# Optimization experiments

Measured on AMD Instinct MI355X. Metric: run time of the kernel, lower is better.

## Reference

```python
import jax, jax.numpy as jnp
import numpy as np


def setup_inputs() -> dict:
    key = jax.random.key(0)
    ks = jax.random.split(key, 8)
    T, B, D = 2048, 8, 1024
    d, NM, k = 64, 8, 2
    Mp1 = NM + 1
    s_in = 1.0 / np.sqrt(D)
    X = jax.random.normal(ks[0], (T, B, D), dtype=jnp.float32)
    M0 = 0.02 * jax.random.normal(ks[1], (d, d), dtype=jnp.float32)
    W_q = s_in * jax.random.normal(ks[2], (D, d), dtype=jnp.float32)
    b_q = jnp.zeros((d,), jnp.float32)
    W_k = s_in * jax.random.normal(ks[3], (D, Mp1 * d), dtype=jnp.float32)
    b_k = jnp.zeros((Mp1 * d,), jnp.float32)
    W_v = s_in * jax.random.normal(ks[4], (D, Mp1 * d), dtype=jnp.float32)
    b_v = jnp.zeros((Mp1 * d,), jnp.float32)
    W_g = s_in * jax.random.normal(ks[5], (D, NM), dtype=jnp.float32)
    b_g = jnp.zeros((NM,), jnp.float32)
    return dict(X=X, M0=M0, W_q=W_q, b_q=b_q, W_k=W_k, b_k=b_k,
                W_v=W_v, b_v=b_v, W_g=W_g, b_g=b_g, k=k)


def _mom_forward(X, M0, W_q, b_q, W_k, b_k, W_v, b_v, W_g, b_g, k):
    T, B, D = X.shape
    d = M0.shape[0]
    NM = W_g.shape[1]
    Mp1 = NM + 1  # memory 0 is the always-on shared memory
    Kp1 = k + 1
    # --- gating + top-k memory selection ---
    scores = jax.nn.softmax(X @ W_g + b_g, axis=-1)               # (T,B,NM)
    m_sc, m_idx = jax.lax.top_k(scores, k)                        # (T,B,k)
    m_sc = m_sc / jnp.sum(m_sc, axis=-1, keepdims=True)
    m_idx = m_idx + 1                                             # shift: 0 reserved for shared memory
    idx_u = jnp.concatenate([jnp.zeros((T, B, 1), m_idx.dtype), m_idx], axis=2)  # (T,B,Kp1)
    sc_u = jnp.concatenate([jnp.ones((T, B, 1), m_sc.dtype), m_sc], axis=2)      # (T,B,Kp1)
    # --- varlen pack: sort replicated tokens by (batch, memory, time) ---
    # NB: the torch build_varlen_pack runs under @torch.no_grad -> detached
    t_rep = jnp.broadcast_to(jnp.arange(T)[:, None, None], (T, B, Kp1)).reshape(-1)
    b_rep = jnp.broadcast_to(jnp.arange(B)[None, :, None], (T, B, Kp1)).reshape(-1)
    m_rep = idx_u.reshape(-1)
    sort_key = b_rep * (Mp1 * T) + m_rep * T + t_rep              # unique per packed token
    perm = jnp.argsort(sort_key)
    t_o = t_rep[perm]
    b_o = b_rep[perm]
    m_id = m_rep[perm]
    alpha = jax.lax.stop_gradient(sc_u.reshape(-1)[perm])         # (Tt,)
    x_tilde = jax.lax.stop_gradient(
        jnp.broadcast_to(X[:, :, None, :], (T, B, Kp1, D)).reshape(-1, D)[perm])  # (Tt,D)
    Tt = T * B * Kp1
    # segment id per packed token; state resets at each new (batch, memory) segment
    seg = b_o * Mp1 + m_id
    new_seg = jnp.concatenate([jnp.ones((1,), bool), seg[1:] != seg[:-1]])
    # --- projections; pick k/v head matching each token's routed memory ---
    q_t = x_tilde @ W_q + b_q                                     # (Tt,d)
    K_all = (x_tilde @ W_k + b_k).reshape(Tt, Mp1, d)
    V_all = (x_tilde @ W_v + b_v).reshape(Tt, Mp1, d)
    k_t = jnp.take_along_axis(K_all, m_id[:, None, None], axis=1)[:, 0]  # (Tt,d)
    v_t = jnp.take_along_axis(V_all, m_id[:, None, None], axis=1)[:, 0]  # (Tt,d)
    # --- per-segment linear-attention recurrence: M_t = M0 + sum k_tau v_tau^T, o_t = q_t @ M_t ---
    def step(M, inp):
        qt, kt, vt, ns = inp
        M = jnp.where(ns, M0, M)
        M = M + kt[:, None] * vt[None, :]
        return M, qt @ M
    _, o_tilde = jax.lax.scan(step, M0, (q_t, k_t, v_t, new_seg))  # (Tt,d)
    # --- weighted scatter-add back to (T,B,d) ---
    o = jnp.zeros((T, B, d), X.dtype).at[t_o, b_o].add(alpha[:, None] * o_tilde)
    return o


def reference(X, M0, W_q, b_q, W_k, b_k, W_v, b_v, W_g, b_g, k):
    return _mom_forward(X, M0, W_q, b_q, W_k, b_k, W_v, b_v, W_g, b_g, k)
```

## Files before the change

kernel.cpp:

```cpp
#include <hip/hip_runtime.h>

#define TT   2048
#define BB   8
#define DD   1024
#define HD   64
#define MP1  9
#define NTOK (TT*BB)
#define CH   64
#define NC   32
#define NSEG (BB*MP1)
#define SEGCAP 2048
#define NCAT 1280
#define LDP  72
#define NZB  1024

typedef __attribute__((ext_vector_type(8))) short bf16x8;
typedef __attribute__((ext_vector_type(4))) float f32x4;

union U8 { uint4 v; unsigned short s[8]; };

static __device__ __forceinline__ unsigned short f2bf(float f) {
  union { float f; unsigned u; } c; c.f = f;
  unsigned r = (c.u + 0x7FFF + ((c.u >> 16) & 1)) >> 16;
  return (unsigned short)r;
}
static __device__ __forceinline__ float bf2f(unsigned short s) {
  union { unsigned u; float f; } c; c.u = ((unsigned)s) << 16;
  return c.f;
}

static __device__ __forceinline__ int sched_walk(
    const int* __restrict__ seglen, int bid, int* chunk_out) {
  const int batch = bid & 7;
  int idx = bid >> 3;
  for (int m = 0; m < MP1; m++) {
    int nch = (seglen[batch * MP1 + m] + 63) >> 6;
    if (idx < nch) { *chunk_out = idx; return batch * MP1 + m; }
    idx -= nch;
  }
  return -1;
}

__global__ __launch_bounds__(256) void prep(
    const float* __restrict__ X,
    const float* __restrict__ Wq, const float* __restrict__ Wk,
    const float* __restrict__ Wv, const float* __restrict__ bq,
    const float* __restrict__ bk, const float* __restrict__ bv,
    const float* __restrict__ Wg, const float* __restrict__ bg,
    unsigned short* __restrict__ Wt, float* __restrict__ bcat,
    int2* __restrict__ idxb, float2* __restrict__ alfb,
    unsigned short* __restrict__ Xb,
    float4* __restrict__ outz, int n4) {
  __shared__ float smem[8 * DD];
  const int tid = threadIdx.x;
  const int id = blockIdx.x;
  if (id >= 1344) {
    int i = (id - 1344) * 256 + tid;
    if (i < n4) outz[i] = make_float4(0.f, 0.f, 0.f, 0.f);
    return;
  }
  if (id < 320) {
    float (*tile)[65] = (float(*)[65])smem;
    const int n0 = (id % 20) * 64, k0 = (id / 20) * 64;
    const int c = tid & 63, rr = tid >> 6;
#pragma unroll 4
    for (int i = 0; i < 16; i++) {
      int kk = k0 + rr * 16 + i;
      int n  = n0 + c;
      float v = 0.f;
      if (n0 < 64)        v = Wq[kk * 64 + n];
      else if (n0 < 640)  v = Wk[kk * 576 + (n - 64)];
      else if (n0 < 1216) v = Wv[kk * 576 + (n - 640)];
      tile[rr * 16 + i][c] = v;
    }
    __syncthreads();
    const int lk = (tid & 15) * 4, ln = tid >> 4;
#pragma unroll
    for (int p = 0; p < 4; p++) {
      int nl = p * 16 + ln;
      ushort4 o;
      o.x = f2bf(tile[lk + 0][nl]); o.y = f2bf(tile[lk + 1][nl]);
      o.z = f2bf(tile[lk + 2][nl]); o.w = f2bf(tile[lk + 3][nl]);
      *(ushort4*)&Wt[(size_t)(n0 + nl) * DD + k0 + lk] = o;
    }
    if (id == 0) {
      for (int idx = tid; idx < NCAT; idx += 256) {
        float b = 0.f;
        if (idx < 64)        b = bq[idx];
        else if (idx < 640)  b = bk[idx - 64];
        else if (idx < 1216) b = bv[idx - 640];
        bcat[idx] = b;
      }
    }
    return;
  }
  float* wgT = smem;
#pragma unroll
  for (int idx4 = tid; idx4 < 2048; idx4 += 256) {
    float4 v = *(const float4*)&Wg[(size_t)idx4 * 4];
    int flat = idx4 * 4;
    int i = flat >> 3, j = flat & 7;
    wgT[(j + 0) * DD + i] = v.x;
    wgT[(j + 1) * DD + i] = v.y;
    wgT[(j + 2) * DD + i] = v.z;
    wgT[(j + 3) * DD + i] = v.w;
  }
  __syncthreads();
  const int lane = tid & 63, wave = tid >> 6;
  const int base_tok = (id - 320) * 16 + wave * 4;
  for (int tk = 0; tk < 4; tk++) {
    const int tok = base_tok + tk;
    const float* xr = X + (size_t)tok * DD;
    unsigned short* xbr = Xb + ((size_t)((tok & 7) * TT + (tok >> 3))) * DD;
    float p[8] = {0.f,0.f,0.f,0.f,0.f,0.f,0.f,0.f};
#pragma unroll
    for (int it = 0; it < 4; it++) {
      int i = it * 256 + lane * 4;
      float4 x = *(const float4*)&xr[i];
      ushort4 o;
      o.x = f2bf(x.x); o.y = f2bf(x.y); o.z = f2bf(x.z); o.w = f2bf(x.w);
      *(ushort4*)&xbr[i] = o;
#pragma unroll
      for (int j = 0; j < 8; j++) {
        float4 wv = *(const float4*)&wgT[j * DD + i];
        p[j] += x.x * wv.x + x.y * wv.y + x.z * wv.z + x.w * wv.w;
      }
    }
#pragma unroll
    for (int j = 0; j < 8; j++) {
      float v = p[j];
#pragma unroll
      for (int off = 32; off > 0; off >>= 1) v += __shfl_xor(v, off);
      p[j] = v + bg[j];
    }
    if (lane == 0) {
      int i1 = 0; float z1 = p[0];
#pragma unroll
      for (int j = 1; j < 8; j++) if (p[j] > z1) { z1 = p[j]; i1 = j; }
      int i2 = -1; float z2 = -3.0e38f;
#pragma unroll
      for (int j = 0; j < 8; j++) if (j != i1 && p[j] > z2) { z2 = p[j]; i2 = j; }
      float e   = expf(z2 - z1);
      float inv = 1.0f / (1.0f + e);
      idxb[tok] = make_int2(i1 + 1, i2 + 1);
      alfb[tok] = make_float2(inv, e * inv);
    }
  }
}

__global__ __launch_bounds__(1024) void pack_kernel(
    const int2* __restrict__ idxb, const float2* __restrict__ alfb,
    int* __restrict__ tlist, float* __restrict__ alist,
    int* __restrict__ seglen) {
  const int seg = blockIdx.x;
  const int b = seg / MP1, m = seg % MP1;
  const int tid = threadIdx.x;
  int* tl = tlist + (size_t)seg * SEGCAP;
  float* al = alist + (size_t)seg * SEGCAP;
  if (m == 0) {
    for (int pos = tid; pos < TT; pos += 1024) { tl[pos] = pos; al[pos] = 1.f; }
    if (tid == 0) seglen[seg] = TT;
    return;
  }
  __shared__ int wsum[16];
  const int lane = tid & 63, w = tid >> 6;
  int base = 0;
  for (int r = 0; r < TT / 1024; r++) {
    int t = r * 1024 + tid;
    int2 ix = idxb[t * BB + b];
    bool f = (ix.x == m || ix.y == m);
    float2 af = alfb[t * BB + b];
    float alpha = (ix.x == m) ? af.x : af.y;
    unsigned long long mask = __ballot(f);
    int lanepos = __popcll(mask & ((1ull << lane) - 1ull));
    if (lane == 0) wsum[w] = __popcll(mask);
    __syncthreads();
    int wbase = 0, total = 0;
#pragma unroll
    for (int i = 0; i < 16; i++) { int v = wsum[i]; if (i < w) wbase += v; total += v; }
    if (f) { int pos = base + wbase + lanepos; tl[pos] = t; al[pos] = alpha; }
    base += total;
    __syncthreads();
  }
  if (tid == 0) seglen[seg] = base;
  int Lpad = (base + 63) & ~63;
  for (int pos = base + tid; pos < Lpad; pos += 1024) { tl[pos] = 0; al[pos] = 0.f; }
}

#define ABUF_H 4096
#define BBUF_H 12288

__global__ __launch_bounds__(256) void pkv_intra(
    const unsigned short* __restrict__ Xb, const unsigned short* __restrict__ Wt,
    const float* __restrict__ bcat,
    const int* __restrict__ tlist, const float* __restrict__ alist,
    const int* __restrict__ seglen,
    unsigned short* __restrict__ Sb16, unsigned short* __restrict__ Qd,
    float* __restrict__ out) {
  int chunk;
  const int seg = sched_walk(seglen, blockIdx.x, &chunk);
  if (seg < 0) return;
  const int t0 = chunk * 64;
  const int L = seglen[seg];
  const int b = seg / MP1, m = seg % MP1;
  __shared__ unsigned short lds[2 * (ABUF_H + BBUF_H)];
  __shared__ int tls[64];
  unsigned short* Asb = lds;
  unsigned short* Bsb = lds + 2 * ABUF_H;
  const int tid = threadIdx.x;
  const int lane = tid & 63, w = tid >> 6;
  if (tid < 64) tls[tid] = tlist[(size_t)seg * SEGCAP + t0 + tid];
  __syncthreads();

  const int lrow = lane >> 2;
  const int lk = (((lane & 3) ^ ((lane >> 3) & 3))) * 8;
  const unsigned short* aPtr = Xb + ((size_t)b * TT + tls[w * 16 + lrow]) * DD + lk;
  const unsigned short* kPtr = Wt + (size_t)(64  + m * 64 + w * 16 + lrow) * DD + lk;
  const unsigned short* vPtr = Wt + (size_t)(640 + m * 64 + w * 16 + lrow) * DD + lk;
  const unsigned short* qPtr = Wt + (size_t)(w * 16 + lrow) * DD + lk;

  const int wr = (w >> 1) * 32;
  const int wc64 = (w & 1);
  const int quad = lane >> 4, l15 = lane & 15;
  const int qs = quad ^ ((l15 >> 1) & 3);

  float biasv[4], qbias[2];
#pragma unroll
  for (int n = 0; n < 4; n++) {
    int col = wc64 * 64 + n * 16 + l15;
    biasv[n] = bcat[col < 64 ? (64 + m * 64 + col) : (640 + m * 64 + (col - 64))];
  }
#pragma unroll
  for (int i = 0; i < 2; i++) qbias[i] = bcat[wc64 * 32 + i * 16 + l15];
  asm volatile("s_waitcnt vmcnt(0)" ::: "memory");
  __builtin_amdgcn_sched_barrier(0);

  f32x4 acc[2][4];
  f32x4 qacc[2][2];
#pragma unroll
  for (int i = 0; i < 2; i++) {
#pragma unroll
    for (int j = 0; j < 4; j++) acc[i][j] = (f32x4){0.f, 0.f, 0.f, 0.f};
#pragma unroll
    for (int j = 0; j < 2; j++) qacc[i][j] = (f32x4){0.f, 0.f, 0.f, 0.f};
  }

#define STG(BUF, K0)                                                             \
  do {                                                                           \
    unsigned short* As_ = Asb + (BUF) * ABUF_H;                                  \
    unsigned short* Bs_ = Bsb + (BUF) * BBUF_H;                                  \
    _Pragma("unroll")                                                            \
    for (int s = 0; s < 2; s++) {                                                \
      __builtin_amdgcn_global_load_lds(                                          \
          (const __attribute__((address_space(1))) unsigned int*)(aPtr + (K0) + s * 32), \
          (__attribute__((address_space(3))) unsigned int*)(As_ + s * 2048 + w * 512),   \
          16, 0, 0);                                                             \
      __builtin_amdgcn_global_load_lds(                                          \
          (const __attribute__((address_space(1))) unsigned int*)(kPtr + (K0) + s * 32), \
          (__attribute__((address_space(3))) unsigned int*)(Bs_ + s * 2048 + w * 512),   \
          16, 0, 0);                                                             \
      __builtin_amdgcn_global_load_lds(                                          \
          (const __attribute__((address_space(1))) unsigned int*)(vPtr + (K0) + s * 32), \
          (__attribute__((address_space(3))) unsigned int*)(Bs_ + 4096 + s * 2048 + w * 512), \
          16, 0, 0);                                                             \
      __builtin_amdgcn_global_load_lds(                                          \
          (const __attribute__((address_space(1))) unsigned int*)(qPtr + (K0) + s * 32), \
          (__attribute__((address_space(3))) unsigned int*)(Bs_ + 8192 + s * 2048 + w * 512), \
          16, 0, 0);                                                             \
    }                                                                            \
  } while (0)

#define CMP(BUF)                                                                 \
  do {                                                                           \
    const unsigned short* As_ = Asb + (BUF) * ABUF_H;                            \
    const unsigned short* Bs_ = Bsb + (BUF) * BBUF_H;                            \
    _Pragma("unroll")                                                            \
    for (int s = 0; s < 2; s++) {                                                \
      bf16x8 af[2], bfr[4];                                                      \
      _Pragma("unroll")                                                          \
      for (int i = 0; i < 2; i++)                                                \
        af[i] = *(const bf16x8*)&As_[s * 2048 + (wr + i * 16 + l15) * 32 + qs * 8]; \
      _Pragma("unroll")                                                          \
      for (int n = 0; n < 4; n++)                                                \
        bfr[n] = *(const bf16x8*)&Bs_[wc64 * 4096 + s * 2048 + (n * 16 + l15) * 32 + qs * 8]; \
      _Pragma("unroll")                                                          \
      for (int mi = 0; mi < 2; mi++)                                             \
        _Pragma("unroll")                                                        \
        for (int ni = 0; ni < 4; ni++)                                           \
          acc[mi][ni] = __builtin_amdgcn_mfma_f32_16x16x32_bf16(af[mi], bfr[ni], acc[mi][ni], 0, 0, 0); \
      {                                                                          \
        bf16x8 qf[2];                                                            \
        _Pragma("unroll")                                                        \
        for (int i = 0; i < 2; i++)                                              \
          qf[i] = *(const bf16x8*)&Bs_[8192 + s * 2048 + (wc64 * 32 + i * 16 + l15) * 32 + qs * 8]; \
        _Pragma("unroll")                                                        \
        for (int mi = 0; mi < 2; mi++)                                           \
          _Pragma("unroll")                                                      \
          for (int ni = 0; ni < 2; ni++)                                         \
            qacc[mi][ni] = __builtin_amdgcn_mfma_f32_16x16x32_bf16(af[mi], qf[ni], qacc[mi][ni], 0, 0, 0); \
      }                                                                          \
    }                                                                            \
  } while (0)

  STG(0, 0);
  STG(1, 64);
  for (int it = 0; it < 15; it++) {
    asm volatile("s_waitcnt vmcnt(8)" ::: "memory");
    __builtin_amdgcn_sched_barrier(0);
    asm volatile("s_barrier" ::: "memory");
    CMP(it & 1);
    asm volatile("s_waitcnt lgkmcnt(0)" ::: "memory");
    __builtin_amdgcn_sched_barrier(0);
    asm volatile("s_barrier" ::: "memory");
    if (it < 14) STG(it & 1, (it + 2) * 64);
  }
  asm volatile("s_waitcnt vmcnt(0)" ::: "memory");
  __builtin_amdgcn_sched_barrier(0);
  asm volatile("s_barrier" ::: "memory");
  CMP(1);
#undef STG
#undef CMP

  asm volatile("s_waitcnt lgkmcnt(0)" ::: "memory");
  __builtin_amdgcn_sched_barrier(0);
  __syncthreads();

  unsigned short* Qs  = lds;
  unsigned short* Ks  = lds + 64 * LDP;
  unsigned short* KTs = lds + 2 * 64 * LDP;
  unsigned short* VTs = lds + 3 * 64 * LDP;

#pragma unroll
  for (int ni = 0; ni < 2; ni++) {
    int qcol = wc64 * 32 + ni * 16 + l15;
#pragma unroll
    for (int mi = 0; mi < 2; mi++) {
#pragma unroll
      for (int r = 0; r < 4; r++) {
        int pr = wr + mi * 16 + quad * 4 + r;
        unsigned short qv = f2bf(qacc[mi][ni][r] + qbias[ni]);
        Qs[pr * LDP + qcol] = qv;
        if (m == 0) Qd[(size_t)((t0 + pr) * BB + b) * HD + qcol] = qv;
      }
    }
  }
#pragma unroll
  for (int ni = 0; ni < 4; ni++) {
    int col = ni * 16 + l15;
#pragma unroll
    for (int mi = 0; mi < 2; mi++) {
#pragma unroll
      for (int r = 0; r < 4; r++) {
        int pr = wr + mi * 16 + quad * 4 + r;
        unsigned short v = f2bf(acc[mi][ni][r] + biasv[ni]);
        if (wc64 == 0) {
          unsigned short kv = (t0 + pr < L) ? v : (unsigned short)0;
          Ks[pr * LDP + col]  = kv;
          KTs[col * LDP + pr] = kv;
        } else {
          VTs[col * LDP + pr] = v;
        }
      }
    }
  }
  __syncthreads();

  const int* tl = tlist + (size_t)seg * SEGCAP;
  {
    const unsigned short* arow = &VTs[(w * 16 + l15) * LDP];
    bf16x8 a0 = *(const bf16x8*)(arow + quad * 8);
    bf16x8 a1 = *(const bf16x8*)(arow + 32 + quad * 8);
    unsigned short* Sp = Sb16 + ((size_t)seg * NC + chunk) * 4096;
#pragma unroll
    for (int n = 0; n < 4; n++) {
      const unsigned short* brow = &KTs[(n * 16 + l15) * LDP];
      f32x4 a2 = __builtin_amdgcn_mfma_f32_16x16x32_bf16(a0, *(const bf16x8*)(brow + quad * 8),
                                                         (f32x4){0.f,0.f,0.f,0.f}, 0, 0, 0);
      a2 = __builtin_amdgcn_mfma_f32_16x16x32_bf16(a1, *(const bf16x8*)(brow + 32 + quad * 8),
                                                   a2, 0, 0, 0);
#pragma unroll
      for (int r = 0; r < 4; r++)
        Sp[(w * 16 + quad * 4 + r) * 64 + n * 16 + l15] = f2bf(a2[r]);
    }
  }
  unsigned short* qrow = &Qs[(w * 16 + l15) * LDP];
  bf16x8 aq0 = *(const bf16x8*)(qrow + quad * 8);
  bf16x8 aq1 = *(const bf16x8*)(qrow + 32 + quad * 8);
  f32x4 pp[4];
#pragma unroll
  for (int n = 0; n < 4; n++) {
    const unsigned short* krow = &Ks[(n * 16 + l15) * LDP];
    pp[n] = __builtin_amdgcn_mfma_f32_16x16x32_bf16(aq0, *(const bf16x8*)(krow + quad * 8),
                                                    (f32x4){0.f,0.f,0.f,0.f}, 0, 0, 0);
    pp[n] = __builtin_amdgcn_mfma_f32_16x16x32_bf16(aq1, *(const bf16x8*)(krow + 32 + quad * 8),
                                                    pp[n], 0, 0, 0);
  }
#pragma unroll
  for (int n = 0; n < 4; n++)
#pragma unroll
    for (int r = 0; r < 4; r++) {
      int i = w * 16 + quad * 4 + r, j = n * 16 + l15;
      Qs[i * LDP + j] = (j <= i) ? f2bf(pp[n][r]) : (unsigned short)0;
    }
  bf16x8 ap0 = *(const bf16x8*)(qrow + quad * 8);
  bf16x8 ap1 = *(const bf16x8*)(qrow + 32 + quad * 8);
  f32x4 po[4];
#pragma unroll
  for (int n = 0; n < 4; n++) {
    const unsigned short* vrow = &VTs[(n * 16 + l15) * LDP];
    po[n] = __builtin_amdgcn_mfma_f32_16x16x32_bf16(ap0, *(const bf16x8*)(vrow + quad * 8),
                                                    (f32x4){0.f,0.f,0.f,0.f}, 0, 0, 0);
    po[n] = __builtin_amdgcn_mfma_f32_16x16x32_bf16(ap1, *(const bf16x8*)(vrow + 32 + quad * 8),
                                                    po[n], 0, 0, 0);
  }
#pragma unroll
  for (int r = 0; r < 4; r++) {
    int pos = t0 + w * 16 + quad * 4 + r;
    if (pos < L) {
      int t = tl[pos];
      float alpha = alist[(size_t)seg * SEGCAP + pos];
#pragma unroll
      for (int n = 0; n < 4; n++)
        atomicAdd(&out[(size_t)(t * BB + b) * HD + n * 16 + l15], alpha * po[n][r]);
    }
  }
}

__global__ __launch_bounds__(256) void scan_kernel(
    const float* __restrict__ M0, const int* __restrict__ seglen,
    unsigned short* __restrict__ Sb16) {
  const int batch = blockIdx.x & 7;
  const int idx = blockIdx.x >> 3;
  const int seg = batch * MP1 + (idx >> 2), slab = idx & 3;
  const int nch = (seglen[seg] + CH - 1) / CH;
  if (nch <= 0) return;
  const int tid = threadIdx.x;
  const int off = slab * 1024 + tid * 4;
  float run[4];
#pragma unroll
  for (int u = 0; u < 4; u++) {
    int o = off + u;
    run[u] = M0[(o & 63) * 64 + (o >> 6)];
  }
  unsigned short* base = Sb16 + (size_t)seg * NC * 4096;
  ushort4 s = *(const ushort4*)(base + off);
  for (int c = 0; c < nch; c++) {
    unsigned short* p = base + c * 4096 + off;
    ushort4 snext;
    if (c + 1 < nch) snext = *(const ushort4*)(p + 4096);
    ushort4 o;
    o.x = f2bf(run[0]); o.y = f2bf(run[1]); o.z = f2bf(run[2]); o.w = f2bf(run[3]);
    *(ushort4*)p = o;
    run[0] += bf2f(s.x); run[1] += bf2f(s.y); run[2] += bf2f(s.z); run[3] += bf2f(s.w);
    s = snext;
  }
}

__global__ __launch_bounds__(256) void chunk_inter(
    const unsigned short* __restrict__ Qd, const unsigned short* __restrict__ Sb16,
    const int* __restrict__ tlist, const float* __restrict__ alist,
    const int* __restrict__ seglen, float* __restrict__ out) {
  int chunk;
  const int seg = sched_walk(seglen, blockIdx.x, &chunk);
  if (seg < 0) return;
  const int L = seglen[seg];
  const int t0 = chunk * CH;
  __shared__ unsigned short Qs[64 * LDP];
  __shared__ unsigned short MT[64 * LDP];
  const int b = seg / MP1;
  const int tid = threadIdx.x;
  const int* tl = tlist + (size_t)seg * SEGCAP;
  {
    int row = tid >> 2, c16 = (tid & 3) << 4;
    int pos = t0 + row;
    const unsigned short* qb = Qd + (size_t)(tl[pos] * BB + b) * HD;
    *(uint4*)&Qs[row * LDP + c16]     = *(const uint4*)(qb + c16);
    *(uint4*)&Qs[row * LDP + c16 + 8] = *(const uint4*)(qb + c16 + 8);
    const unsigned short* Mp = Sb16 + ((size_t)seg * NC + chunk) * 4096 + row * 64 + c16;
    *(uint4*)&MT[row * LDP + c16]     = *(const uint4*)(Mp);
    *(uint4*)&MT[row * LDP + c16 + 8] = *(const uint4*)(Mp + 8);
  }
  __syncthreads();
  const int lane = tid & 63, w = tid >> 6;
  const int quad = lane >> 4, l15 = lane & 15;
  const unsigned short* qrow = &Qs[(w * 16 + l15) * LDP];
  bf16x8 aq0 = *(const bf16x8*)(qrow + quad * 8);
  bf16x8 aq1 = *(const bf16x8*)(qrow + 32 + quad * 8);
  f32x4 po[4];
#pragma unroll
  for (int n = 0; n < 4; n++) {
    const unsigned short* mrow = &MT[(n * 16 + l15) * LDP];
    po[n] = __builtin_amdgcn_mfma_f32_16x16x32_bf16(aq0, *(const bf16x8*)(mrow + quad * 8),
                                                    (f32x4){0.f,0.f,0.f,0.f}, 0, 0, 0);
    po[n] = __builtin_amdgcn_mfma_f32_16x16x32_bf16(aq1, *(const bf16x8*)(mrow + 32 + quad * 8),
                                                    po[n], 0, 0, 0);
  }
#pragma unroll
  for (int r = 0; r < 4; r++) {
    int pos = t0 + w * 16 + quad * 4 + r;
    if (pos < L) {
      int t = tl[pos];
      float alpha = alist[(size_t)seg * SEGCAP + pos];
#pragma unroll
      for (int n = 0; n < 4; n++)
        atomicAdd(&out[(size_t)(t * BB + b) * HD + n * 16 + l15], alpha * po[n][r]);
    }
  }
}

extern "C" void kernel_launch(void* const* d_in, const int* in_sizes, int n_in,
                              void* d_out, int out_size, void* d_ws, size_t ws_size,
                              hipStream_t stream) {
  const float* X  = (const float*)d_in[0];
  const float* M0 = (const float*)d_in[1];
  const float* Wq = (const float*)d_in[2];
  const float* bq = (const float*)d_in[3];
  const float* Wk = (const float*)d_in[4];
  const float* bk = (const float*)d_in[5];
  const float* Wv = (const float*)d_in[6];
  const float* bv = (const float*)d_in[7];
  const float* Wg = (const float*)d_in[8];
  const float* bg = (const float*)d_in[9];

  char* ws = (char*)d_ws;
  unsigned short* Xb   = (unsigned short*)(ws);
  unsigned short* Wt   = (unsigned short*)(ws + 33554432ULL);
  float*          bcat = (float*)         (ws + 36175872ULL);
  unsigned short* Qd   = (unsigned short*)(ws + 36180992ULL);
  unsigned short* Sb16 = (unsigned short*)(ws + 76026880ULL);
  int2*           idxb = (int2*)          (ws + 94901248ULL);
  float2*         alfb = (float2*)        (ws + 95032320ULL);
  int*            tlist= (int*)           (ws + 95163392ULL);
  float*          alist= (float*)         (ws + 95753216ULL);
  int*            slen = (int*)           (ws + 96343040ULL);

  float* out = (float*)d_out;
  const int n4 = out_size / 4;

  prep<<<320 + NTOK / 16 + NZB, 256, 0, stream>>>(
      X, Wq, Wk, Wv, bq, bk, bv, Wg, bg, Wt, bcat, idxb, alfb, Xb,
      (float4*)out, n4);
  pack_kernel<<<NSEG, 1024, 0, stream>>>(idxb, alfb, tlist, alist, slen);
  pkv_intra<<<1024, 256, 0, stream>>>(Xb, Wt, bcat, tlist, alist, slen, Sb16, Qd, out);
  scan_kernel<<<288, 256, 0, stream>>>(M0, slen, Sb16);
  chunk_inter<<<1024, 256, 0, stream>>>(Qd, Sb16, tlist, alist, slen, out);
}
```

Baseline: 110.9 us.

## Double pkv_intra block to 512 threads, splitting GEMM rows across eight waves

Launches the projection/intra-chunk kernel with 8 waves instead of 4. Each wave now computes a 16-row slice of the K/V/Q projection instead of 32 rows. Each wave also stages one of the four source arrays (X, K, V or Q weights) into shared memory, and the vmcnt wait drops to match the smaller number of loads in flight per wave. The intra-chunk attention epilogue stays on the first four waves. This halves per-wave accumulator registers and raises the number of waves available to hide latency, at the cost of idle waves in the epilogue and more barrier participants.

```diff
diff --git a/kernel.cpp b/kernel.cpp
--- a/kernel.cpp
+++ b/kernel.cpp
@@ -190,7 +190,7 @@
 #define ABUF_H 4096
 #define BBUF_H 12288
 
-__global__ __launch_bounds__(256) void pkv_intra(
+__global__ __launch_bounds__(512) void pkv_intra(
     const unsigned short* __restrict__ Xb, const unsigned short* __restrict__ Wt,
     const float* __restrict__ bcat,
     const int* __restrict__ tlist, const float* __restrict__ alist,
@@ -212,17 +212,26 @@
   if (tid < 64) tls[tid] = tlist[(size_t)seg * SEGCAP + t0 + tid];
   __syncthreads();
 
-  const int lrow = lane >> 2;
-  const int lk = (((lane & 3) ^ ((lane >> 3) & 3))) * 8;
-  const unsigned short* aPtr = Xb + ((size_t)b * TT + tls[w * 16 + lrow]) * DD + lk;
-  const unsigned short* kPtr = Wt + (size_t)(64  + m * 64 + w * 16 + lrow) * DD + lk;
-  const unsigned short* vPtr = Wt + (size_t)(640 + m * 64 + w * 16 + lrow) * DD + lk;
-  const unsigned short* qPtr = Wt + (size_t)(w * 16 + lrow) * DD + lk;
-
-  const int wr = (w >> 1) * 32;
-  const int wc64 = (w & 1);
+  const int arr = w >> 1;
+  const int sl  = w & 1;
+  const int lk  = (((lane & 3) ^ ((lane >> 3) & 3))) * 8;
+  const unsigned short* src[4];
+#pragma unroll
+  for (int i = 0; i < 4; i++) {
+    int row = i * 16 + (lane >> 2);
+    const unsigned short* p;
+    if (arr == 0)      p = Xb + ((size_t)b * TT + tls[row]) * DD;
+    else if (arr == 1) p = Wt + (size_t)(64  + m * 64 + row) * DD;
+    else if (arr == 2) p = Wt + (size_t)(640 + m * 64 + row) * DD;
+    else               p = Wt + (size_t)(row) * DD;
+    src[i] = p + sl * 32 + lk;
+  }
+  const int dstoff = (arr == 0) ? (sl * 2048) : ((arr - 1) * 4096 + sl * 2048);
+
+  const int wrB  = (w >> 1) * 16;
+  const int wc64 = w & 1;
   const int quad = lane >> 4, l15 = lane & 15;
-  const int qs = quad ^ ((l15 >> 1) & 3);
+  const int qs   = quad ^ ((l15 >> 1) & 3);
 
   float biasv[4], qbias[2];
 #pragma unroll
@@ -235,39 +244,23 @@
   asm volatile("s_waitcnt vmcnt(0)" ::: "memory");
   __builtin_amdgcn_sched_barrier(0);
 
-  f32x4 acc[2][4];
-  f32x4 qacc[2][2];
-#pragma unroll
-  for (int i = 0; i < 2; i++) {
-#pragma unroll
-    for (int j = 0; j < 4; j++) acc[i][j] = (f32x4){0.f, 0.f, 0.f, 0.f};
-#pragma unroll
-    for (int j = 0; j < 2; j++) qacc[i][j] = (f32x4){0.f, 0.f, 0.f, 0.f};
-  }
+  f32x4 acc[4];
+  f32x4 qacc[2];
+#pragma unroll
+  for (int j = 0; j < 4; j++) acc[j] = (f32x4){0.f, 0.f, 0.f, 0.f};
+#pragma unroll
+  for (int j = 0; j < 2; j++) qacc[j] = (f32x4){0.f, 0.f, 0.f, 0.f};
 
 #define STG(BUF, K0)                                                             \
   do {                                                                           \
-    unsigned short* As_ = Asb + (BUF) * ABUF_H;                                  \
-    unsigned short* Bs_ = Bsb + (BUF) * BBUF_H;                                  \
+    unsigned short* db = ((arr == 0) ? (Asb + (BUF) * ABUF_H)                    \
+                                     : (Bsb + (BUF) * BBUF_H)) + dstoff;         \
     _Pragma("unroll")                                                            \
-    for (int s = 0; s < 2; s++) {                                                \
+    for (int i = 0; i < 4; i++)                                                  \
       __builtin_amdgcn_global_load_lds(                                          \
-          (const __attribute__((address_space(1))) unsigned int*)(aPtr + (K0) + s * 32), \
-          (__attribute__((address_space(3))) unsigned int*)(As_ + s * 2048 + w * 512),   \
+          (const __attribute__((address_space(1))) unsigned int*)(src[i] + (K0)),\
+          (__attribute__((address_space(3))) unsigned int*)(db + i * 512),       \
           16, 0, 0);                                                             \
-      __builtin_amdgcn_global_load_lds(                                          \
-          (const __attribute__((address_space(1))) unsigned int*)(kPtr + (K0) + s * 32), \
-          (__attribute__((address_space(3))) unsigned int*)(Bs_ + s * 2048 + w * 512),   \
-          16, 0, 0);                                                             \
-      __builtin_amdgcn_global_load_lds(                                          \
-          (const __attribute__((address_space(1))) unsigned int*)(vPtr + (K0) + s * 32), \
-          (__attribute__((address_space(3))) unsigned int*)(Bs_ + 4096 + s * 2048 + w * 512), \
-          16, 0, 0);                                                             \
-      __builtin_amdgcn_global_load_lds(                                          \
-          (const __attribute__((address_space(1))) unsigned int*)(qPtr + (K0) + s * 32), \
-          (__attribute__((address_space(3))) unsigned int*)(Bs_ + 8192 + s * 2048 + w * 512), \
-          16, 0, 0);                                                             \
-    }                                                                            \
   } while (0)
 
 #define CMP(BUF)                                                                 \
@@ -276,28 +269,22 @@
     const unsigned short* Bs_ = Bsb + (BUF) * BBUF_H;                            \
     _Pragma("unroll")                                                            \
     for (int s = 0; s < 2; s++) {                                                \
-      bf16x8 af[2], bfr[4];                                                      \
-      _Pragma("unroll")                                                          \
-      for (int i = 0; i < 2; i++)                                                \
-        af[i] = *(const bf16x8*)&As_[s * 2048 + (wr + i * 16 + l15) * 32 + qs * 8]; \
+      bf16x8 af = *(const bf16x8*)&As_[s * 2048 + (wrB + l15) * 32 + qs * 8];    \
+      bf16x8 bfr[4];                                                             \
       _Pragma("unroll")                                                          \
       for (int n = 0; n < 4; n++)                                                \
         bfr[n] = *(const bf16x8*)&Bs_[wc64 * 4096 + s * 2048 + (n * 16 + l15) * 32 + qs * 8]; \
       _Pragma("unroll")                                                          \
-      for (int mi = 0; mi < 2; mi++)                                             \
-        _Pragma("unroll")                                                        \
-        for (int ni = 0; ni < 4; ni++)                                           \
-          acc[mi][ni] = __builtin_amdgcn_mfma_f32_16x16x32_bf16(af[mi], bfr[ni], acc[mi][ni], 0, 0, 0); \
+      for (int ni = 0; ni < 4; ni++)                                             \
+        acc[ni] = __builtin_amdgcn_mfma_f32_16x16x32_bf16(af, bfr[ni], acc[ni], 0, 0, 0); \
       {                                                                          \
         bf16x8 qf[2];                                                            \
         _Pragma("unroll")                                                        \
         for (int i = 0; i < 2; i++)                                              \
           qf[i] = *(const bf16x8*)&Bs_[8192 + s * 2048 + (wc64 * 32 + i * 16 + l15) * 32 + qs * 8]; \
         _Pragma("unroll")                                                        \
-        for (int mi = 0; mi < 2; mi++)                                           \
-          _Pragma("unroll")                                                      \
-          for (int ni = 0; ni < 2; ni++)                                         \
-            qacc[mi][ni] = __builtin_amdgcn_mfma_f32_16x16x32_bf16(af[mi], qf[ni], qacc[mi][ni], 0, 0, 0); \
+        for (int ni = 0; ni < 2; ni++)                                           \
+          qacc[ni] = __builtin_amdgcn_mfma_f32_16x16x32_bf16(af, qf[ni], qacc[ni], 0, 0, 0); \
       }                                                                          \
     }                                                                            \
   } while (0)
@@ -305,7 +292,7 @@
   STG(0, 0);
   STG(1, 64);
   for (int it = 0; it < 15; it++) {
-    asm volatile("s_waitcnt vmcnt(8)" ::: "memory");
+    asm volatile("s_waitcnt vmcnt(4)" ::: "memory");
     __builtin_amdgcn_sched_barrier(0);
     asm volatile("s_barrier" ::: "memory");
     CMP(it & 1);
@@ -334,94 +321,90 @@
   for (int ni = 0; ni < 2; ni++) {
     int qcol = wc64 * 32 + ni * 16 + l15;
 #pragma unroll
-    for (int mi = 0; mi < 2; mi++) {
-#pragma unroll
-      for (int r = 0; r < 4; r++) {
-        int pr = wr + mi * 16 + quad * 4 + r;
-        unsigned short qv = f2bf(qacc[mi][ni][r] + qbias[ni]);
-        Qs[pr * LDP + qcol] = qv;
-        if (m == 0) Qd[(size_t)((t0 + pr) * BB + b) * HD + qcol] = qv;
-      }
+    for (int r = 0; r < 4; r++) {
+      int pr = wrB + quad * 4 + r;
+      unsigned short qv = f2bf(qacc[ni][r] + qbias[ni]);
+      Qs[pr * LDP + qcol] = qv;
+      if (m == 0) Qd[(size_t)((t0 + pr) * BB + b) * HD + qcol] = qv;
     }
   }
 #pragma unroll
   for (int ni = 0; ni < 4; ni++) {
     int col = ni * 16 + l15;
 #pragma unroll
-    for (int mi = 0; mi < 2; mi++) {
+    for (int r = 0; r < 4; r++) {
+      int pr = wrB + quad * 4 + r;
+      unsigned short v = f2bf(acc[ni][r] + biasv[ni]);
+      if (wc64 == 0) {
+        unsigned short kv = (t0 + pr < L) ? v : (unsigned short)0;
+        Ks[pr * LDP + col]  = kv;
+        KTs[col * LDP + pr] = kv;
+      } else {
+        VTs[col * LDP + pr] = v;
+      }
+    }
+  }
+  __syncthreads();
+
+  if (w < 4) {
+    const int* tl = tlist + (size_t)seg * SEGCAP;
+    {
+      const unsigned short* arow = &VTs[(w * 16 + l15) * LDP];
+      bf16x8 a0 = *(const bf16x8*)(arow + quad * 8);
+      bf16x8 a1 = *(const bf16x8*)(arow + 32 + quad * 8);
+      unsigned short* Sp = Sb16 + ((size_t)seg * NC + chunk) * 4096;
+#pragma unroll
+      for (int n = 0; n < 4; n++) {
+        const unsigned short* brow = &KTs[(n * 16 + l15) * LDP];
+        f32x4 a2 = __builtin_amdgcn_mfma_f32_16x16x32_bf16(a0, *(const bf16x8*)(brow + quad * 8),
+                                                           (f32x4){0.f,0.f,0.f,0.f}, 0, 0, 0);
+        a2 = __builtin_amdgcn_mfma_f32_16x16x32_bf16(a1, *(const bf16x8*)(brow + 32 + quad * 8),
+                                                     a2, 0, 0, 0);
+#pragma unroll
+        for (int r = 0; r < 4; r++)
+          Sp[(w * 16 + quad * 4 + r) * 64 + n * 16 + l15] = f2bf(a2[r]);
+      }
+    }
+    unsigned short* qrow = &Qs[(w * 16 + l15) * LDP];
+    bf16x8 aq0 = *(const bf16x8*)(qrow + quad * 8);
+    bf16x8 aq1 = *(const bf16x8*)(qrow + 32 + quad * 8);
+    f32x4 pp[4];
+#pragma unroll
+    for (int n = 0; n < 4; n++) {
+      const unsigned short* krow = &Ks[(n * 16 + l15) * LDP];
+      pp[n] = __builtin_amdgcn_mfma_f32_16x16x32_bf16(aq0, *(const bf16x8*)(krow + quad * 8),
+                                                      (f32x4){0.f,0.f,0.f,0.f}, 0, 0, 0);
+      pp[n] = __builtin_amdgcn_mfma_f32_16x16x32_bf16(aq1, *(const bf16x8*)(krow + 32 + quad * 8),
+                                                      pp[n], 0, 0, 0);
+    }
+#pragma unroll
+    for (int n = 0; n < 4; n++)
 #pragma unroll
       for (int r = 0; r < 4; r++) {
-        int pr = wr + mi * 16 + quad * 4 + r;
-        unsigned short v = f2bf(acc[mi][ni][r] + biasv[ni]);
-        if (wc64 == 0) {
-          unsigned short kv = (t0 + pr < L) ? v : (unsigned short)0;
-          Ks[pr * LDP + col]  = kv;
-          KTs[col * LDP + pr] = kv;
-        } else {
-          VTs[col * LDP + pr] = v;
-        }
+        int i = w * 16 + quad * 4 + r, j = n * 16 + l15;
+        Qs[i * LDP + j] = (j <= i) ? f2bf(pp[n][r]) : (unsigned short)0;
       }
-    }
-  }
-  __syncthreads();
-
-  const int* tl = tlist + (size_t)seg * SEGCAP;
-  {
-    const unsigned short* arow = &VTs[(w * 16 + l15) * LDP];
-    bf16x8 a0 = *(const bf16x8*)(arow + quad * 8);
-    bf16x8 a1 = *(const bf16x8*)(arow + 32 + quad * 8);
-    unsigned short* Sp = Sb16 + ((size_t)seg * NC + chunk) * 4096;
+    bf16x8 ap0 = *(const bf16x8*)(qrow + quad * 8);
+    bf16x8 ap1 = *(const bf16x8*)(qrow + 32 + quad * 8);
+    f32x4 po[4];
 #pragma unroll
     for (int n = 0; n < 4; n++) {
-      const unsigned short* brow = &KTs[(n * 16 + l15) * LDP];
-      f32x4 a2 = __builtin_amdgcn_mfma_f32_16x16x32_bf16(a0, *(const bf16x8*)(brow + quad * 8),
-                                                         (f32x4){0.f,0.f,0.f,0.f}, 0, 0, 0);
-      a2 = __builtin_amdgcn_mfma_f32_16x16x32_bf16(a1, *(const bf16x8*)(brow + 32 + quad * 8),
-                                                   a2, 0, 0, 0);
-#pragma unroll
-      for (int r = 0; r < 4; r++)
-        Sp[(w * 16 + quad * 4 + r) * 64 + n * 16 + l15] = f2bf(a2[r]);
-    }
-  }
-  unsigned short* qrow = &Qs[(w * 16 + l15) * LDP];
-  bf16x8 aq0 = *(const bf16x8*)(qrow + quad * 8);
-  bf16x8 aq1 = *(const bf16x8*)(qrow + 32 + quad * 8);
-  f32x4 pp[4];
-#pragma unroll
-  for (int n = 0; n < 4; n++) {
-    const unsigned short* krow = &Ks[(n * 16 + l15) * LDP];
-    pp[n] = __builtin_amdgcn_mfma_f32_16x16x32_bf16(aq0, *(const bf16x8*)(krow + quad * 8),
-                                                    (f32x4){0.f,0.f,0.f,0.f}, 0, 0, 0);
-    pp[n] = __builtin_amdgcn_mfma_f32_16x16x32_bf16(aq1, *(const bf16x8*)(krow + 32 + quad * 8),
-                                                    pp[n], 0, 0, 0);
-  }
-#pragma unroll
-  for (int n = 0; n < 4; n++)
+      const unsigned short* vrow = &VTs[(n * 16 + l15) * LDP];
+      po[n] = __builtin_amdgcn_mfma_f32_16x16x32_bf16(ap0, *(const bf16x8*)(vrow + quad * 8),
+                                                      (f32x4){0.f,0.f,0.f,0.f}, 0, 0, 0);
+      po[n] = __builtin_amdgcn_mfma_f32_16x16x32_bf16(ap1, *(const bf16x8*)(vrow + 32 + quad * 8),
+                                                      po[n], 0, 0, 0);
+    }
 #pragma unroll
     for (int r = 0; r < 4; r++) {
-      int i = w * 16 + quad * 4 + r, j = n * 16 + l15;
-      Qs[i * LDP + j] = (j <= i) ? f2bf(pp[n][r]) : (unsigned short)0;
-    }
-  bf16x8 ap0 = *(const bf16x8*)(qrow + quad * 8);
-  bf16x8 ap1 = *(const bf16x8*)(qrow + 32 + quad * 8);
-  f32x4 po[4];
-#pragma unroll
-  for (int n = 0; n < 4; n++) {
-    const unsigned short* vrow = &VTs[(n * 16 + l15) * LDP];
-    po[n] = __builtin_amdgcn_mfma_f32_16x16x32_bf16(ap0, *(const bf16x8*)(vrow + quad * 8),
-                                                    (f32x4){0.f,0.f,0.f,0.f}, 0, 0, 0);
-    po[n] = __builtin_amdgcn_mfma_f32_16x16x32_bf16(ap1, *(const bf16x8*)(vrow + 32 + quad * 8),
-                                                    po[n], 0, 0, 0);
-  }
-#pragma unroll
-  for (int r = 0; r < 4; r++) {
-    int pos = t0 + w * 16 + quad * 4 + r;
-    if (pos < L) {
-      int t = tl[pos];
-      float alpha = alist[(size_t)seg * SEGCAP + pos];
-#pragma unroll
-      for (int n = 0; n < 4; n++)
-        atomicAdd(&out[(size_t)(t * BB + b) * HD + n * 16 + l15], alpha * po[n][r]);
+      int pos = t0 + w * 16 + quad * 4 + r;
+      if (pos < L) {
+        int t = tl[pos];
+        float alpha = alist[(size_t)seg * SEGCAP + pos];
+#pragma unroll
+        for (int n = 0; n < 4; n++)
+          atomicAdd(&out[(size_t)(t * BB + b) * HD + n * 16 + l15], alpha * po[n][r]);
+      }
     }
   }
 }
@@ -541,7 +524,7 @@
       X, Wq, Wk, Wv, bq, bk, bv, Wg, bg, Wt, bcat, idxb, alfb, Xb,
       (float4*)out, n4);
   pack_kernel<<<NSEG, 1024, 0, stream>>>(idxb, alfb, tlist, alist, slen);
-  pkv_intra<<<1024, 256, 0, stream>>>(Xb, Wt, bcat, tlist, alist, slen, Sb16, Qd, out);
+  pkv_intra<<<1024, 512, 0, stream>>>(Xb, Wt, bcat, tlist, alist, slen, Sb16, Qd, out);
   scan_kernel<<<288, 256, 0, stream>>>(M0, slen, Sb16);
   chunk_inter<<<1024, 256, 0, stream>>>(Qd, Sb16, tlist, alist, slen, out);
 }
```

Result: faster. 104.1 us (-6.1%).
